# Kernel tuning notes

Measured on AMD Instinct MI355X. Metric: run time of the kernel, lower is better.

## Reference

```python
import jax, jax.numpy as jnp
import numpy as np
import math

B, C_IN, H, W = 1, 3, 96, 96
FEAT_C, GDIM, BLOCK = 64, 8, 16
TW, TH = (W + BLOCK - 1) // BLOCK, (H + BLOCK - 1) // BLOCK
TWO_PI = 2.0 * math.pi
EPS = 1e-6


def setup_inputs() -> dict:
    key = jax.random.key(0)
    ks = jax.random.split(key, 3)
    inp = jax.random.normal(ks[0], (B, C_IN, H, W), jnp.float32)
    w_enc = jax.random.normal(ks[1], (FEAT_C, C_IN, 3, 3), jnp.float32) / np.sqrt(C_IN * 9).astype(np.float32)
    b_enc = jnp.zeros((FEAT_C,), jnp.float32)
    w_head = jax.random.normal(ks[2], (GDIM, FEAT_C), jnp.float32) / np.sqrt(FEAT_C).astype(np.float32)
    b_head = jnp.zeros((GDIM,), jnp.float32)
    return {"inp": inp, "w_enc": w_enc, "b_enc": b_enc, "w_head": w_head, "b_head": b_head}


def _rasterize_one(rgb, scale, theta, x_ndc, y_ndc):
    # rgb (N,3), scale (N,2), theta (N,), x_ndc/y_ndc (N,) ; N = H*W gaussians
    c, s = jnp.cos(theta), jnp.sin(theta)
    v0, v1 = scale[:, 0] ** 2, scale[:, 1] ** 2
    # Sigma = R diag(s)^2 R^T
    S00 = c * c * v0 + s * s * v1
    S01 = c * s * (v0 - v1)
    S11 = s * s * v0 + c * c * v1
    det = S00 * S11 - S01 * S01
    inv_det = 1.0 / det
    ca, cb, cc = S11 * inv_det, -S01 * inv_det, S00 * inv_det  # conic (a,b,c)
    bmid = 0.5 * (S00 + S11)
    lam1 = bmid + jnp.sqrt(jnp.maximum(0.1, bmid * bmid - det))
    radius = jax.lax.stop_gradient(jnp.ceil(3.0 * jnp.sqrt(lam1)))
    # ndc -> pixel centers
    cx = 0.5 * W * (x_ndc + 1.0) - 0.5
    cy = 0.5 * H * (y_ndc + 1.0) - 0.5
    cxs, cys = jax.lax.stop_gradient(cx), jax.lax.stop_gradient(cy)
    # tile bbox (C-style trunc-toward-zero casts, matching the CUDA kernel)
    tmin_x = jnp.clip(((cxs - radius) / BLOCK).astype(jnp.int32), 0, TW)
    tmax_x = jnp.clip(((cxs + radius) / BLOCK).astype(jnp.int32) + 1, 0, TW)
    tmin_y = jnp.clip(((cys - radius) / BLOCK).astype(jnp.int32), 0, TH)
    tmax_y = jnp.clip(((cys + radius) / BLOCK).astype(jnp.int32) + 1, 0, TH)
    # pixel grid, row-major (i over H, j over W); P = H*W
    prow, pcol = jnp.meshgrid(jnp.arange(H), jnp.arange(W), indexing='ij')
    px = pcol.reshape(-1).astype(jnp.float32)
    py = prow.reshape(-1).astype(jnp.float32)
    tx = (pcol.reshape(-1) // BLOCK).astype(jnp.int32)
    ty = (prow.reshape(-1) // BLOCK).astype(jnp.int32)
    dx = cx[:, None] - px[None, :]  # (N,P)
    dy = cy[:, None] - py[None, :]
    sigma = 0.5 * (ca[:, None] * dx * dx + cc[:, None] * dy * dy) + cb[:, None] * dx * dy
    alpha = jnp.minimum(0.999, jnp.exp(-sigma))  # opacity == 1
    valid = ((sigma >= 0.0) & (alpha >= 1.0 / 255.0)
             & (radius[:, None] > 0)
             & (tx[None, :] >= tmin_x[:, None]) & (tx[None, :] < tmax_x[:, None])
             & (ty[None, :] >= tmin_y[:, None]) & (ty[None, :] < tmax_y[:, None]))
    wgt = jnp.where(valid, alpha, 0.0)
    out = jnp.einsum('np,nc->pc', wgt, rgb)  # order-independent sum compositing
    return out.reshape(H, W, 3).transpose(2, 0, 1)  # (3,H,W)


def _forward(inp, w_enc, b_enc, w_head, b_head):
    Bn = inp.shape[0]
    feat = jax.lax.conv_general_dilated(
        inp, w_enc, (1, 1), 'SAME',
        dimension_numbers=('NCHW', 'OIHW', 'NCHW')) + b_enc[None, :, None, None]
    pred = jnp.einsum('bchw,oc->bhwo', feat, w_head) + b_head  # 1x1 head
    pred = pred.reshape(Bn, H * W, GDIM)
    rgb = pred[..., 0:3]
    theta = jax.nn.sigmoid(pred[..., 3]) * TWO_PI
    scale = jax.nn.sigmoid(pred[..., 4:6]) * 0.5 + EPS
    offset = jnp.tanh(pred[..., 6:8])
    # get_coord(h_inp, w_inp): coord[...,0] varies over width, coord[...,1] over height
    xg = (2.0 * jnp.arange(H, dtype=jnp.float32) / H - 1.0)[:, None]
    yg = (2.0 * jnp.arange(W, dtype=jnp.float32) / W - 1.0)[None, :]
    coord0 = jnp.broadcast_to(yg, (H, W)).reshape(-1)
    coord1 = jnp.broadcast_to(xg, (H, W)).reshape(-1)
    x_ndc = coord0[None, :] + 2.0 * offset[..., 0] / W - 1.0 / W
    y_ndc = coord1[None, :] + 2.0 * offset[..., 1] / H - 1.0 / H
    img = jax.vmap(_rasterize_one)(rgb, scale, theta, x_ndc, y_ndc)
    return jnp.clip(img, 0.0, 1.0)  # (B,3,H,W)


def reference(inp, w_enc, b_enc, w_head, b_head):
    return _forward(inp, w_enc, b_enc, w_head, b_head)
```

## Files before the change

kernel.cpp:

```cpp
#include <hip/hip_runtime.h>
#include <math.h>

#define HH   96
#define WW   96
#define NPIX 9216
#define TWT  6
#define THT  6
#define SW   24
#define NSRC (SW*SW)

__device__ __forceinline__ float fast_sigmoid(float x) {
    return 1.0f / (1.0f + __expf(-x));
}
__device__ __forceinline__ float fast_tanh(float x) {
    return 1.0f - 2.0f / (__expf(2.0f * x) + 1.0f);
}

__global__ __launch_bounds__(256) void gauss_fused_kernel(
    const float* __restrict__ inp, const float* __restrict__ w_enc,
    const float* __restrict__ b_enc, const float* __restrict__ w_head,
    const float* __restrict__ b_head, float* __restrict__ out)
{
    __shared__ float  wcomb[8][27];
    __shared__ float  bcomb[8];
    __shared__ float4 lgA[NSRC];
    __shared__ float4 lgB[NSRC];
    __shared__ int    lgb[NSRC];

    const int tid = threadIdx.x;
    const int bx = blockIdx.x % 6, by = blockIdx.x / 6;
    const int r0 = by * 16, c0 = bx * 16;
    const int sr0 = r0 - 3, sc0 = c0 - 3;

    if (tid < 216) {
        const int o = tid / 27, r = tid % 27;
        float acc = 0.0f;
        for (int c = 0; c < 64; ++c)
            acc = fmaf(w_head[o * 64 + c], w_enc[c * 27 + r], acc);
        wcomb[o][r] = acc;
    } else if (tid < 224) {
        const int o = tid - 216;
        float acc = b_head[o];
        for (int c = 0; c < 64; ++c)
            acc = fmaf(w_head[o * 64 + c], b_enc[c], acc);
        bcomb[o] = acc;
    }
    __syncthreads();

    for (int s = tid; s < NSRC; s += 256) {
        const int sr = s / SW, sc = s - sr * SW;
        const int gr = sr0 + sr, gc = sc0 + sc;
        if (gr < 0 || gr >= HH || gc < 0 || gc >= WW) continue;

        float pred[8];
        #pragma unroll
        for (int o = 0; o < 8; ++o) pred[o] = bcomb[o];
        #pragma unroll
        for (int i = 0; i < 3; ++i) {
            #pragma unroll
            for (int dy = 0; dy < 3; ++dy) {
                const int y = gr + dy - 1;
                #pragma unroll
                for (int dx = 0; dx < 3; ++dx) {
                    const int x = gc + dx - 1;
                    float v = 0.0f;
                    if (y >= 0 && y < HH && x >= 0 && x < WW)
                        v = inp[i * NPIX + y * WW + x];
                    const int r = (i * 3 + dy) * 3 + dx;
                    #pragma unroll
                    for (int o = 0; o < 8; ++o)
                        pred[o] = fmaf(wcomb[o][r], v, pred[o]);
                }
            }
        }

        const float theta = fast_sigmoid(pred[3]) * 6.28318530717958647692f;
        const float cth = __cosf(theta), sth = __sinf(theta);
        const float s0 = fast_sigmoid(pred[4]) * 0.5f + 1e-6f;
        const float s1 = fast_sigmoid(pred[5]) * 0.5f + 1e-6f;
        const float v0 = s0 * s0, v1 = s1 * s1;
        const float S00 = cth * cth * v0 + sth * sth * v1;
        const float S01 = cth * sth * (v0 - v1);
        const float S11 = sth * sth * v0 + cth * cth * v1;
        const float det = S00 * S11 - S01 * S01;
        const float inv_det = 1.0f / det;
        const float ca = S11 * inv_det;
        const float cb = -S01 * inv_det;
        const float cc = S00 * inv_det;
        const float bmid = 0.5f * (S00 + S11);
        const float lam1 = bmid + sqrtf(fmaxf(0.1f, bmid * bmid - det));
        const float radius = ceilf(3.0f * sqrtf(lam1));
        const float off0 = fast_tanh(pred[6]);
        const float off1 = fast_tanh(pred[7]);
        const float coord0 = 2.0f * (float)gc / (float)WW - 1.0f;
        const float coord1 = 2.0f * (float)gr / (float)HH - 1.0f;
        const float x_ndc = coord0 + 2.0f * off0 / (float)WW - 1.0f / (float)WW;
        const float y_ndc = coord1 + 2.0f * off1 / (float)HH - 1.0f / (float)HH;
        const float cx = 0.5f * (float)WW * (x_ndc + 1.0f) - 0.5f;
        const float cy = 0.5f * (float)HH * (y_ndc + 1.0f) - 0.5f;

        int tminx = (int)((cx - radius) / 16.0f);
        int tmaxx = (int)((cx + radius) / 16.0f) + 1;
        int tminy = (int)((cy - radius) / 16.0f);
        int tmaxy = (int)((cy + radius) / 16.0f) + 1;
        tminx = min(max(tminx, 0), TWT); tmaxx = min(max(tmaxx, 0), TWT);
        tminy = min(max(tminy, 0), THT); tmaxy = min(max(tmaxy, 0), THT);
        if (!(radius > 0.0f)) { tmaxx = tminx; tmaxy = tminy; }

        lgA[s] = make_float4(cx, cy, ca, cb);
        lgB[s] = make_float4(cc, pred[0], pred[1], pred[2]);
        lgb[s] = tminx | (tmaxx << 8) | (tminy << 16) | (tmaxy << 24);
    }
    __syncthreads();

    const int lr = tid >> 4, lc = tid & 15;
    const int row = r0 + lr, col = c0 + lc;
    const int tx = col >> 4, ty = row >> 4;
    const float px = (float)col, py = (float)row;

    float aR = 0.0f, aG = 0.0f, aB = 0.0f;
    #pragma unroll
    for (int wr = 0; wr < 9; ++wr) {
        const int gr = row - 3 + wr;
        if (gr < 0 || gr >= HH) continue;
        const int sbase = (lr + wr) * SW + lc;
        for (int wc = 0; wc < 9; ++wc) {
            const int gc = col - 3 + wc;
            if (gc < 0 || gc >= WW) continue;
            const int s = sbase + wc;
            const float4 A  = lgA[s];
            const float4 Bv = lgB[s];
            const float dx = A.x - px;
            const float dy = A.y - py;
            const float sigma = 0.5f * (A.z * dx * dx + Bv.x * dy * dy) + A.w * dx * dy;
            const float alpha = fminf(0.999f, __expf(-sigma));
            const int bnd = lgb[s];
            const bool valid = (sigma >= 0.0f) && (alpha >= (1.0f / 255.0f)) &&
                               (tx >= (bnd & 0xff)) && (tx < ((bnd >> 8) & 0xff)) &&
                               (ty >= ((bnd >> 16) & 0xff)) && (ty < ((bnd >> 24) & 0xff));
            if (valid) {
                aR = fmaf(alpha, Bv.y, aR);
                aG = fmaf(alpha, Bv.z, aG);
                aB = fmaf(alpha, Bv.w, aB);
            }
        }
    }
    const int p = row * WW + col;
    out[0 * NPIX + p] = fminf(fmaxf(aR, 0.0f), 1.0f);
    out[1 * NPIX + p] = fminf(fmaxf(aG, 0.0f), 1.0f);
    out[2 * NPIX + p] = fminf(fmaxf(aB, 0.0f), 1.0f);
}

extern "C" void kernel_launch(void* const* d_in, const int* in_sizes, int n_in,
                              void* d_out, int out_size, void* d_ws, size_t ws_size,
                              hipStream_t stream)
{
    const float* inp    = (const float*)d_in[0];
    const float* w_enc  = (const float*)d_in[1];
    const float* b_enc  = (const float*)d_in[2];
    const float* w_head = (const float*)d_in[3];
    const float* b_head = (const float*)d_in[4];
    float* out = (float*)d_out;

    gauss_fused_kernel<<<36, 256, 0, stream>>>(inp, w_enc, b_enc, w_head, b_head, out);
}
```

Before: 79.25 us.

## Shrink blocks to 2-row strips and split each pixel's 9x9 window across 8 lanes

The launch grows from 36 blocks to 288. Each block now covers a 2x16 pixel strip with a 10x24 halo of gaussian sources, so every thread computes at most one source. In the splat phase, 8 lanes share one pixel, each taking a slice of the 81 window entries, and the partial sums are combined with xor shuffles. The goal is to fill far more of the GPU's compute units than 36 blocks can. The cost is more halo recomputation, since rows overlap between strips, and every block redoes the 64-channel weight fold.

```diff
diff --git a/kernel.cpp b/kernel.cpp
--- a/kernel.cpp
+++ b/kernel.cpp
@@ -6,8 +6,9 @@
 #define NPIX 9216
 #define TWT  6
 #define THT  6
-#define SW   24
-#define NSRC (SW*SW)
+#define SWC  24
+#define SWR  10
+#define NSRC (SWR*SWC)
 
 __device__ __forceinline__ float fast_sigmoid(float x) {
     return 1.0f / (1.0f + __expf(-x));
@@ -28,8 +29,9 @@
     __shared__ int    lgb[NSRC];
 
     const int tid = threadIdx.x;
-    const int bx = blockIdx.x % 6, by = blockIdx.x / 6;
-    const int r0 = by * 16, c0 = bx * 16;
+    const int bx = blockIdx.x % 6;
+    const int rp = blockIdx.x / 6;
+    const int r0 = rp * 2, c0 = bx * 16;
     const int sr0 = r0 - 3, sc0 = c0 - 3;
 
     if (tid < 216) {
@@ -47,108 +49,113 @@
     }
     __syncthreads();
 
-    for (int s = tid; s < NSRC; s += 256) {
-        const int sr = s / SW, sc = s - sr * SW;
+    if (tid < NSRC) {
+        const int sr = tid / SWC, sc = tid - sr * SWC;
         const int gr = sr0 + sr, gc = sc0 + sc;
-        if (gr < 0 || gr >= HH || gc < 0 || gc >= WW) continue;
-
-        float pred[8];
-        #pragma unroll
-        for (int o = 0; o < 8; ++o) pred[o] = bcomb[o];
-        #pragma unroll
-        for (int i = 0; i < 3; ++i) {
+        if (gr >= 0 && gr < HH && gc >= 0 && gc < WW) {
+            float pred[8];
             #pragma unroll
-            for (int dy = 0; dy < 3; ++dy) {
-                const int y = gr + dy - 1;
+            for (int o = 0; o < 8; ++o) pred[o] = bcomb[o];
+            #pragma unroll
+            for (int i = 0; i < 3; ++i) {
                 #pragma unroll
-                for (int dx = 0; dx < 3; ++dx) {
-                    const int x = gc + dx - 1;
-                    float v = 0.0f;
-                    if (y >= 0 && y < HH && x >= 0 && x < WW)
-                        v = inp[i * NPIX + y * WW + x];
-                    const int r = (i * 3 + dy) * 3 + dx;
+                for (int dy = 0; dy < 3; ++dy) {
+                    const int y = gr + dy - 1;
                     #pragma unroll
-                    for (int o = 0; o < 8; ++o)
-                        pred[o] = fmaf(wcomb[o][r], v, pred[o]);
+                    for (int dx = 0; dx < 3; ++dx) {
+                        const int x = gc + dx - 1;
+                        float v = 0.0f;
+                        if (y >= 0 && y < HH && x >= 0 && x < WW)
+                            v = inp[i * NPIX + y * WW + x];
+                        const int r = (i * 3 + dy) * 3 + dx;
+                        #pragma unroll
+                        for (int o = 0; o < 8; ++o)
+                            pred[o] = fmaf(wcomb[o][r], v, pred[o]);
+                    }
                 }
             }
+
+            const float theta = fast_sigmoid(pred[3]) * 6.28318530717958647692f;
+            const float cth = __cosf(theta), sth = __sinf(theta);
+            const float s0 = fast_sigmoid(pred[4]) * 0.5f + 1e-6f;
+            const float s1 = fast_sigmoid(pred[5]) * 0.5f + 1e-6f;
+            const float v0 = s0 * s0, v1 = s1 * s1;
+            const float S00 = cth * cth * v0 + sth * sth * v1;
+            const float S01 = cth * sth * (v0 - v1);
+            const float S11 = sth * sth * v0 + cth * cth * v1;
+            const float det = S00 * S11 - S01 * S01;
+            const float inv_det = 1.0f / det;
+            const float ca = S11 * inv_det;
+            const float cb = -S01 * inv_det;
+            const float cc = S00 * inv_det;
+            const float bmid = 0.5f * (S00 + S11);
+            const float lam1 = bmid + sqrtf(fmaxf(0.1f, bmid * bmid - det));
+            const float radius = ceilf(3.0f * sqrtf(lam1));
+            const float off0 = fast_tanh(pred[6]);
+            const float off1 = fast_tanh(pred[7]);
+            const float coord0 = 2.0f * (float)gc / (float)WW - 1.0f;
+            const float coord1 = 2.0f * (float)gr / (float)HH - 1.0f;
+            const float x_ndc = coord0 + 2.0f * off0 / (float)WW - 1.0f / (float)WW;
+            const float y_ndc = coord1 + 2.0f * off1 / (float)HH - 1.0f / (float)HH;
+            const float cx = 0.5f * (float)WW * (x_ndc + 1.0f) - 0.5f;
+            const float cy = 0.5f * (float)HH * (y_ndc + 1.0f) - 0.5f;
+
+            int tminx = (int)((cx - radius) / 16.0f);
+            int tmaxx = (int)((cx + radius) / 16.0f) + 1;
+            int tminy = (int)((cy - radius) / 16.0f);
+            int tmaxy = (int)((cy + radius) / 16.0f) + 1;
+            tminx = min(max(tminx, 0), TWT); tmaxx = min(max(tmaxx, 0), TWT);
+            tminy = min(max(tminy, 0), THT); tmaxy = min(max(tmaxy, 0), THT);
+            if (!(radius > 0.0f)) { tmaxx = tminx; tmaxy = tminy; }
+
+            lgA[tid] = make_float4(cx, cy, ca, cb);
+            lgB[tid] = make_float4(cc, pred[0], pred[1], pred[2]);
+            lgb[tid] = tminx | (tmaxx << 8) | (tminy << 16) | (tmaxy << 24);
         }
-
-        const float theta = fast_sigmoid(pred[3]) * 6.28318530717958647692f;
-        const float cth = __cosf(theta), sth = __sinf(theta);
-        const float s0 = fast_sigmoid(pred[4]) * 0.5f + 1e-6f;
-        const float s1 = fast_sigmoid(pred[5]) * 0.5f + 1e-6f;
-        const float v0 = s0 * s0, v1 = s1 * s1;
-        const float S00 = cth * cth * v0 + sth * sth * v1;
-        const float S01 = cth * sth * (v0 - v1);
-        const float S11 = sth * sth * v0 + cth * cth * v1;
-        const float det = S00 * S11 - S01 * S01;
-        const float inv_det = 1.0f / det;
-        const float ca = S11 * inv_det;
-        const float cb = -S01 * inv_det;
-        const float cc = S00 * inv_det;
-        const float bmid = 0.5f * (S00 + S11);
-        const float lam1 = bmid + sqrtf(fmaxf(0.1f, bmid * bmid - det));
-        const float radius = ceilf(3.0f * sqrtf(lam1));
-        const float off0 = fast_tanh(pred[6]);
-        const float off1 = fast_tanh(pred[7]);
-        const float coord0 = 2.0f * (float)gc / (float)WW - 1.0f;
-        const float coord1 = 2.0f * (float)gr / (float)HH - 1.0f;
-        const float x_ndc = coord0 + 2.0f * off0 / (float)WW - 1.0f / (float)WW;
-        const float y_ndc = coord1 + 2.0f * off1 / (float)HH - 1.0f / (float)HH;
-        const float cx = 0.5f * (float)WW * (x_ndc + 1.0f) - 0.5f;
-        const float cy = 0.5f * (float)HH * (y_ndc + 1.0f) - 0.5f;
-
-        int tminx = (int)((cx - radius) / 16.0f);
-        int tmaxx = (int)((cx + radius) / 16.0f) + 1;
-        int tminy = (int)((cy - radius) / 16.0f);
-        int tmaxy = (int)((cy + radius) / 16.0f) + 1;
-        tminx = min(max(tminx, 0), TWT); tmaxx = min(max(tmaxx, 0), TWT);
-        tminy = min(max(tminy, 0), THT); tmaxy = min(max(tmaxy, 0), THT);
-        if (!(radius > 0.0f)) { tmaxx = tminx; tmaxy = tminy; }
-
-        lgA[s] = make_float4(cx, cy, ca, cb);
-        lgB[s] = make_float4(cc, pred[0], pred[1], pred[2]);
-        lgb[s] = tminx | (tmaxx << 8) | (tminy << 16) | (tmaxy << 24);
     }
     __syncthreads();
 
-    const int lr = tid >> 4, lc = tid & 15;
+    const int pix   = tid >> 3;
+    const int slice = tid & 7;
+    const int lr = pix >> 4, lc = pix & 15;
     const int row = r0 + lr, col = c0 + lc;
     const int tx = col >> 4, ty = row >> 4;
     const float px = (float)col, py = (float)row;
 
     float aR = 0.0f, aG = 0.0f, aB = 0.0f;
     #pragma unroll
-    for (int wr = 0; wr < 9; ++wr) {
+    for (int idx = slice; idx < 81; idx += 8) {
+        const int wr = idx / 9, wc = idx - wr * 9;
         const int gr = row - 3 + wr;
-        if (gr < 0 || gr >= HH) continue;
-        const int sbase = (lr + wr) * SW + lc;
-        for (int wc = 0; wc < 9; ++wc) {
-            const int gc = col - 3 + wc;
-            if (gc < 0 || gc >= WW) continue;
-            const int s = sbase + wc;
-            const float4 A  = lgA[s];
-            const float4 Bv = lgB[s];
-            const float dx = A.x - px;
-            const float dy = A.y - py;
-            const float sigma = 0.5f * (A.z * dx * dx + Bv.x * dy * dy) + A.w * dx * dy;
-            const float alpha = fminf(0.999f, __expf(-sigma));
-            const int bnd = lgb[s];
-            const bool valid = (sigma >= 0.0f) && (alpha >= (1.0f / 255.0f)) &&
-                               (tx >= (bnd & 0xff)) && (tx < ((bnd >> 8) & 0xff)) &&
-                               (ty >= ((bnd >> 16) & 0xff)) && (ty < ((bnd >> 24) & 0xff));
-            if (valid) {
-                aR = fmaf(alpha, Bv.y, aR);
-                aG = fmaf(alpha, Bv.z, aG);
-                aB = fmaf(alpha, Bv.w, aB);
-            }
+        const int gc = col - 3 + wc;
+        if (gr < 0 || gr >= HH || gc < 0 || gc >= WW) continue;
+        const int s = (lr + wr) * SWC + (lc + wc);
+        const float4 A  = lgA[s];
+        const float4 Bv = lgB[s];
+        const float dx = A.x - px;
+        const float dy = A.y - py;
+        const float sigma = 0.5f * (A.z * dx * dx + Bv.x * dy * dy) + A.w * dx * dy;
+        const float alpha = fminf(0.999f, __expf(-sigma));
+        const int bnd = lgb[s];
+        const bool valid = (sigma >= 0.0f) && (alpha >= (1.0f / 255.0f)) &&
+                           (tx >= (bnd & 0xff)) && (tx < ((bnd >> 8) & 0xff)) &&
+                           (ty >= ((bnd >> 16) & 0xff)) && (ty < ((bnd >> 24) & 0xff));
+        if (valid) {
+            aR = fmaf(alpha, Bv.y, aR);
+            aG = fmaf(alpha, Bv.z, aG);
+            aB = fmaf(alpha, Bv.w, aB);
         }
     }
-    const int p = row * WW + col;
-    out[0 * NPIX + p] = fminf(fmaxf(aR, 0.0f), 1.0f);
-    out[1 * NPIX + p] = fminf(fmaxf(aG, 0.0f), 1.0f);
-    out[2 * NPIX + p] = fminf(fmaxf(aB, 0.0f), 1.0f);
+
+    aR += __shfl_xor(aR, 1); aR += __shfl_xor(aR, 2); aR += __shfl_xor(aR, 4);
+    aG += __shfl_xor(aG, 1); aG += __shfl_xor(aG, 2); aG += __shfl_xor(aG, 4);
+    aB += __shfl_xor(aB, 1); aB += __shfl_xor(aB, 2); aB += __shfl_xor(aB, 4);
+
+    if (slice < 3) {
+        const int p = row * WW + col;
+        const float v = (slice == 0) ? aR : (slice == 1) ? aG : aB;
+        out[slice * NPIX + p] = fminf(fmaxf(v, 0.0f), 1.0f);
+    }
 }
 
 extern "C" void kernel_launch(void* const* d_in, const int* in_sizes, int n_in,
@@ -162,5 +169,5 @@
     const float* b_head = (const float*)d_in[4];
     float* out = (float*)d_out;
 
-    gauss_fused_kernel<<<36, 256, 0, stream>>>(inp, w_enc, b_enc, w_head, b_head, out);
+    gauss_fused_kernel<<<288, 256, 0, stream>>>(inp, w_enc, b_enc, w_head, b_head, out);
 }
```

Result: faster. 74.07 us (-6.5%).
